# Performance work log

Measured on AMD Instinct MI355X. Metric: run time of the kernel, lower is better.

Reference implementation:

```python
import jax, jax.numpy as jnp
import numpy as np

N, E, D, H, C = 100000, 1600000, 64, 8, 10
NEG_SLOPE = 0.2


def setup_inputs() -> dict:
    key = jax.random.key(0)
    ks = jax.random.split(key, 20)
    rn = lambda k, sh: jax.random.normal(k, sh, jnp.float32) * 0.1
    return dict(
        x=jax.random.normal(ks[0], (N, D), jnp.float32),
        edge_index=jax.random.randint(ks[1], (2, E), 0, N),
        gcnK_W=rn(ks[2], (D, D)), gcnK_b=rn(ks[3], (D,)),
        gcnV_W=rn(ks[4], (D, D)), gcnV_b=rn(ks[5], (D,)),
        super_Q=rn(ks[6], (C, D)),
        mha_in_w=rn(ks[7], (3 * D, D)), mha_in_b=rn(ks[8], (3 * D,)),
        mha_out_w=rn(ks[9], (D, D)), mha_out_b=rn(ks[10], (D,)),
        gat_W=rn(ks[11], (D, D)), gat_Wc=rn(ks[12], (D, D)),
        gat_a_src=rn(ks[13], (D,)), gat_a_dst=rn(ks[14], (D,)),
        gat_b=rn(ks[15], (D,)),
        t1_W=rn(ks[16], (D, 2 * D)), t1_b=rn(ks[17], (2 * D,)),
        t2_W=rn(ks[18], (2 * D, D)), t2_b=rn(ks[19], (D,)),
    )


def _gcn(x, W, b, src, dst, norm_e):
    # PyG GCNConv: symmetric-normalized aggregation over (A + I)
    h = x @ W  # [N, D]
    agg = jax.ops.segment_sum(h[src] * norm_e[:, None], dst, num_segments=N)
    return agg + b


def _mha(q, k, v, in_w, in_b, out_w, out_b):
    # torch.nn.MultiheadAttention (unbatched), eval mode (dropout off)
    L, n, hd = q.shape[0], k.shape[0], D // H
    Wq, Wk, Wv = jnp.split(in_w, 3, axis=0)
    bq, bk, bv = jnp.split(in_b, 3)
    scale = 1.0 / float(np.sqrt(hd))
    qh = ((q @ Wq.T + bq) * scale).reshape(L, H, hd).transpose(1, 0, 2)  # [H,L,hd]
    kh = (k @ Wk.T + bk).reshape(n, H, hd).transpose(1, 0, 2)            # [H,n,hd]
    vh = (v @ Wv.T + bv).reshape(n, H, hd).transpose(1, 0, 2)
    attn = jax.nn.softmax(jnp.einsum('hld,hnd->hln', qh, kh), axis=-1)
    o = jnp.einsum('hln,hnd->hld', attn, vh).transpose(1, 0, 2).reshape(L, D)
    return o @ out_w.T + out_b


def _context_gat(x, src, dst, context, W, Wc, a_src, a_dst, b):
    # context-conditioned GAT: per-edge logits use node terms + global context gate
    h = x @ W
    c = context @ Wc  # [D]
    s_src = h @ (a_src + c)  # context modulates source attention vector
    s_dst = h @ a_dst
    logits = jax.nn.leaky_relu(s_src[src] + s_dst[dst], NEG_SLOPE)  # [E]
    m = jax.ops.segment_max(logits, dst, num_segments=N)
    ex = jnp.exp(logits - m[dst])
    denom = jax.ops.segment_sum(ex, dst, num_segments=N)
    alpha = ex / (denom[dst] + 1e-16)
    out = jax.ops.segment_sum(alpha[:, None] * h[src], dst, num_segments=N)
    return out + b


def reference(x, edge_index, gcnK_W, gcnK_b, gcnV_W, gcnV_b, super_Q,
              mha_in_w, mha_in_b, mha_out_w, mha_out_b,
              gat_W, gat_Wc, gat_a_src, gat_a_dst, gat_b,
              t1_W, t1_b, t2_W, t2_b):
    src, dst = edge_index[0], edge_index[1]
    loop = jnp.arange(N)
    srcl = jnp.concatenate([src, loop])
    dstl = jnp.concatenate([dst, loop])
    deg = jax.ops.segment_sum(jnp.ones_like(srcl, jnp.float32), dstl, num_segments=N)
    dinv = jnp.where(deg > 0, 1.0 / jnp.sqrt(deg), 0.0)
    norm_e = dinv[srcl] * dinv[dstl]
    x_K = _gcn(x, gcnK_W, gcnK_b, srcl, dstl, norm_e)
    x_V = _gcn(x, gcnV_W, gcnV_b, srcl, dstl, norm_e)
    cluster = _mha(super_Q, x_K, x_V, mha_in_w, mha_in_b, mha_out_w, mha_out_b)  # [C, D]
    context = jnp.mean(cluster, axis=0)  # [D]
    g = _context_gat(x_V, src, dst, context, gat_W, gat_Wc, gat_a_src, gat_a_dst, gat_b)
    h1 = jax.nn.relu(g @ t1_W + t1_b)
    return jax.nn.relu(h1 @ t2_W + t2_b)
```

## Files before the change

### kernel.cpp

```cpp
#include <hip/hip_runtime.h>
#include <hip/hip_bf16.h>
#include <stdint.h>

#define NN 100000
#define EE 1600000
#define NBK 391
#define CHUNK 4096
#define NCB 98
#define NPROJ 1563
#define NS 32

typedef __attribute__((ext_vector_type(8))) short bf16x8;
typedef __attribute__((ext_vector_type(4))) float f32x4;
typedef __attribute__((ext_vector_type(2))) float f32x2;
union FragU { uint4 u; bf16x8 h; };

__device__ inline unsigned pack_bf2(float a, float b) {
  __hip_bfloat162 t;
  t.x = __float2bfloat16(a);
  t.y = __float2bfloat16(b);
  return *reinterpret_cast<unsigned*>(&t);
}

__device__ inline f32x2 unpk2(unsigned u) {
  f32x2 r;
  r.x = __uint_as_float(u << 16);
  r.y = __uint_as_float(u & 0xffff0000u);
  return r;
}

__launch_bounds__(256)
__global__ void k_hist(const int* __restrict__ ei, int* __restrict__ histmat) {
  __shared__ int hist[NCB];
  int t = threadIdx.x;
  if (t < NCB) hist[t] = 0;
  __syncthreads();
  int base = blockIdx.x * CHUNK;
  int nb = EE - base; if (nb > CHUNK) nb = CHUNK;
  for (int k = t; k < nb; k += 256)
    atomicAdd(&hist[ei[EE + base + k] >> 10], 1);
  __syncthreads();
  if (t < NCB) histmat[blockIdx.x * NCB + t] = hist[t];
}

__launch_bounds__(256)
__global__ void k_sumcb(const int* __restrict__ histmat, int* __restrict__ cbsum) {
  __shared__ int red[4];
  int cb = blockIdx.x, t = threadIdx.x;
  int s = 0;
  for (int blk = t; blk < NBK; blk += 256) s += histmat[blk * NCB + cb];
#pragma unroll
  for (int off = 32; off > 0; off >>= 1) s += __shfl_down(s, off);
  if ((t & 63) == 0) red[t >> 6] = s;
  __syncthreads();
  if (t == 0) cbsum[cb] = red[0] + red[1] + red[2] + red[3];
}

__launch_bounds__(512)
__global__ void k_ppos(const int* __restrict__ histmat, const int* __restrict__ cbsum,
                       int* __restrict__ bstart, int* __restrict__ offsets,
                       int* __restrict__ ppos) {
  __shared__ int sm[512];
  __shared__ int sb[128];
  int cb = blockIdx.x, t = threadIdx.x;
  if (t < 128) sb[t] = (t < NCB) ? cbsum[t] : 0;
  __syncthreads();
  for (int off = 1; off < 128; off <<= 1) {
    int x = (t < 128 && t >= off) ? sb[t - off] : 0;
    __syncthreads();
    if (t < 128) sb[t] += x;
    __syncthreads();
  }
  int bs = (cb == 0) ? 0 : sb[cb - 1];
  if (t == 0) bstart[cb] = bs;
  if (cb == 0 && t == 0) { bstart[NCB] = EE; offsets[NN] = EE; }
  int v = (t < NBK) ? histmat[t * NCB + cb] : 0;
  sm[t] = v;
  __syncthreads();
  for (int off = 1; off < 512; off <<= 1) {
    int x = (t >= off) ? sm[t - off] : 0;
    __syncthreads();
    sm[t] += x;
    __syncthreads();
  }
  if (t < NBK) ppos[cb * NBK + t] = bs + sm[t] - v;
}

__launch_bounds__(256)
__global__ void k_fill_b(const int* __restrict__ ei, const int* __restrict__ ppos,
                         unsigned* __restrict__ brec) {
  __shared__ int hist[NCB], binstart[NCB], bincur[NCB], pbase[NCB];
  __shared__ unsigned lbuf[CHUNK];
  __shared__ unsigned char cbArr[CHUNK];
  int t = threadIdx.x;
  int base = blockIdx.x * CHUNK;
  int nb = EE - base; if (nb > CHUNK) nb = CHUNK;
  if (t < NCB) { hist[t] = 0; pbase[t] = ppos[t * NBK + blockIdx.x]; }
  __syncthreads();
  unsigned rec[16]; int rcb[16]; int cnt = 0;
  for (int k = t; k < nb; k += 256) {
    int s = ei[base + k], d = ei[EE + base + k];
    rec[cnt] = (unsigned)s | ((unsigned)(d & 1023) << 17);
    rcb[cnt] = d >> 10;
    atomicAdd(&hist[rcb[cnt]], 1);
    cnt++;
  }
  __syncthreads();
  if (t < NCB) binstart[t] = hist[t];
  __syncthreads();
  for (int off = 1; off < NCB; off <<= 1) {
    int v = (t < NCB && t >= off) ? binstart[t - off] : 0;
    __syncthreads();
    if (t < NCB) binstart[t] += v;
    __syncthreads();
  }
  if (t < NCB) { binstart[t] -= hist[t]; bincur[t] = 0; }
  __syncthreads();
  for (int i = 0; i < cnt; i++) {
    int c = rcb[i];
    int pos = atomicAdd(&bincur[c], 1);
    int p = binstart[c] + pos;
    lbuf[p] = rec[i];
    cbArr[p] = (unsigned char)c;
  }
  __syncthreads();
  for (int i = t; i < nb; i += 256) {
    int c = cbArr[i];
    brec[pbase[c] + (i - binstart[c])] = lbuf[i];
  }
}

__launch_bounds__(1024)
__global__ void k_fill_c(const unsigned* __restrict__ brec, const int* __restrict__ bstart,
                         int* __restrict__ csr, int* __restrict__ offsets,
                         float* __restrict__ dinv) {
  __shared__ int cnt[1024], sm[1024];
  int cbk = blockIdx.x, t = threadIdx.x;
  int nb0 = cbk << 10;
  int nn = NN - nb0; if (nn > 1024) nn = 1024;
  cnt[t] = 0;
  __syncthreads();
  int e0 = bstart[cbk], e1 = bstart[cbk + 1];
  for (int j = e0 + t; j < e1; j += 1024)
    atomicAdd(&cnt[brec[j] >> 17], 1);
  __syncthreads();
  int cv = cnt[t];
  sm[t] = cv;
  __syncthreads();
  for (int off = 1; off < 1024; off <<= 1) {
    int v = (t >= off) ? sm[t - off] : 0;
    __syncthreads();
    sm[t] += v;
    __syncthreads();
  }
  sm[t] -= cv;
  if (t < nn) {
    offsets[nb0 + t] = e0 + sm[t];
    dinv[nb0 + t] = rsqrtf((float)(cv + 1));
  }
  cnt[t] = 0;
  __syncthreads();
  for (int j = e0 + t; j < e1; j += 1024) {
    unsigned r = brec[j];
    int dl = r >> 17;
    int p = atomicAdd(&cnt[dl], 1);
    csr[e0 + sm[dl] + p] = r & 0x1FFFF;
  }
}

__global__ void k_prep(const float* __restrict__ x, const float* __restrict__ dinv,
                       unsigned* __restrict__ xbf2) {
  int i = blockIdx.x * 256 + threadIdx.x;
  if (i >= NN * 32) return;
  float dv = dinv[i >> 5];
  float2 v = ((const float2*)x)[i];
  xbf2[i] = pack_bf2(v.x * dv, v.y * dv);
}

__launch_bounds__(256)
__global__ void k_agg_x(const unsigned* __restrict__ xbf2, const int* __restrict__ offsets,
                        const int* __restrict__ csr, const float* __restrict__ dinv,
                        unsigned* __restrict__ axb) {
  int gid = blockIdx.x * 256 + threadIdx.x;
  int n = gid >> 6;
  if (n >= NN) return;
  int lane = gid & 63, q = lane & 7, grp = lane >> 3;
  int e0 = offsets[n], e1 = offsets[n + 1];
  float dv = dinv[n];
  f32x2 a2[4];
#pragma unroll
  for (int i = 0; i < 4; i++) a2[i] = (f32x2){0.f, 0.f};
  if (grp == 0) {
    uint4 u = ((const uint4*)(xbf2 + (size_t)n * 32))[q];
    unsigned uu[4] = {u.x, u.y, u.z, u.w};
#pragma unroll
    for (int p = 0; p < 4; p++) a2[p] += unpk2(uu[p]);
  }
  int b2 = e0;
  for (; b2 + 8 < e1; b2 += 16) {
    int j0 = b2 + grp, j1 = j0 + 8;
    int s0 = csr[j0];
    bool ok1 = j1 < e1;
    int s1 = ok1 ? csr[j1] : s0;
    uint4 u0 = ((const uint4*)(xbf2 + (size_t)s0 * 32))[q];
    uint4 u1 = ((const uint4*)(xbf2 + (size_t)s1 * 32))[q];
    unsigned w0[4] = {u0.x, u0.y, u0.z, u0.w};
    unsigned w1[4] = {u1.x, u1.y, u1.z, u1.w};
#pragma unroll
    for (int p = 0; p < 4; p++) a2[p] += unpk2(w0[p]);
    if (ok1) {
#pragma unroll
      for (int p = 0; p < 4; p++) a2[p] += unpk2(w1[p]);
    }
  }
  for (; b2 < e1; b2 += 8) {
    int j = b2 + grp;
    if (j < e1) {
      int s = csr[j];
      uint4 u = ((const uint4*)(xbf2 + (size_t)s * 32))[q];
      unsigned uu[4] = {u.x, u.y, u.z, u.w};
#pragma unroll
      for (int p = 0; p < 4; p++) a2[p] += unpk2(uu[p]);
    }
  }
#pragma unroll
  for (int i = 0; i < 4; i++) {
    a2[i].x += __shfl_xor(a2[i].x, 8);
    a2[i].x += __shfl_xor(a2[i].x, 16);
    a2[i].x += __shfl_xor(a2[i].x, 32);
    a2[i].y += __shfl_xor(a2[i].y, 8);
    a2[i].y += __shfl_xor(a2[i].y, 16);
    a2[i].y += __shfl_xor(a2[i].y, 32);
  }
  if (lane < 8) {
    uint4 u;
    u.x = pack_bf2(a2[0].x * dv, a2[0].y * dv);
    u.y = pack_bf2(a2[1].x * dv, a2[1].y * dv);
    u.z = pack_bf2(a2[2].x * dv, a2[2].y * dv);
    u.w = pack_bf2(a2[3].x * dv, a2[3].y * dv);
    ((uint4*)(axb + (size_t)n * 32))[q] = u;
  }
}

__launch_bounds__(256)
__global__ void k_fusew(const float* __restrict__ gcnK_W, const float* __restrict__ gcnK_b,
                        const float* __restrict__ gcnV_W, const float* __restrict__ gcnV_b,
                        const float* __restrict__ mha_in_w, const float* __restrict__ mha_in_b,
                        const float* __restrict__ gat_W, const float* __restrict__ sQ,
                        const float* __restrict__ t1W, const float* __restrict__ t2W,
                        unsigned* __restrict__ Wt, float* __restrict__ bb,
                        unsigned* __restrict__ W1b, unsigned* __restrict__ W2b) {
  __shared__ float sW1[64 * 65];
  __shared__ float sW2[64 * 65];
  __shared__ float sW3[64 * 65];
  __shared__ float sqq[640], qhs[640], Ms[5120], kb[64];
  int blk = blockIdx.x, t = threadIdx.x;
  const float scale = 0.35355339059327373f;
  if (blk < 16) {
    for (int i = t; i < 4096; i += 256) sW1[(i >> 6) * 65 + (i & 63)] = gcnV_W[i];
    if (blk < 8) {
      for (int i = t; i < 512; i += 256) sW2[i] = mha_in_w[(128 + blk * 8) * 64 + i];
    } else {
      for (int i = t; i < 4096; i += 256) sW2[(i >> 6) * 65 + (i & 63)] = gat_W[i];
    }
    __syncthreads();
    int idx = blk * 256 + t;
    int d = idx >> 5, kp = idx & 31;
    float v2[2];
#pragma unroll
    for (int u2 = 0; u2 < 2; u2++) {
      int k = kp * 2 + u2;
      float s = 0.f;
      if (d < 64) {
        int r = d & 7;
        for (int j = 0; j < 64; j++) s = fmaf(sW1[k * 65 + j], sW2[r * 64 + j], s);
      } else {
        int c = d - 64;
        for (int j = 0; j < 64; j++) s = fmaf(sW1[k * 65 + j], sW2[j * 65 + c], s);
      }
      v2[u2] = s;
    }
    Wt[idx] = pack_bf2(v2[0], v2[1]);
    if (t < 8) {
      if (blk < 8) {
        int d0 = blk * 8 + t;
        float s = mha_in_b[128 + d0];
        for (int j = 0; j < 64; j++) s = fmaf(gcnV_b[j], sW2[t * 64 + j], s);
        bb[d0] = s;
      } else {
        int c = (blk - 8) * 8 + t;
        float s = 0.f;
        for (int j = 0; j < 64; j++) s = fmaf(gcnV_b[j], sW2[j * 65 + c], s);
        bb[64 + c] = s;
      }
    }
  } else if (blk == 16) {
    for (int i = t; i < 4096; i += 256) {
      int r = i >> 6, c = i & 63;
      sW1[r * 65 + c] = gcnK_W[i];
      sW2[r * 65 + c] = mha_in_w[64 * 64 + i];
      sW3[r * 65 + c] = mha_in_w[i];
    }
    for (int i = t; i < 640; i += 256) sqq[i] = sQ[i];
    __syncthreads();
    for (int e = t; e < 640; e += 256) {
      int lv = e >> 6, c = e & 63;
      float acc = mha_in_b[c];
      for (int i = 0; i < 64; i++) acc = fmaf(sqq[lv * 64 + i], sW3[c * 65 + i], acc);
      qhs[e] = acc * scale;
    }
    if (t < 64) {
      float s = mha_in_b[64 + t];
      for (int j = 0; j < 64; j++) s = fmaf(gcnK_b[j], sW2[t * 65 + j], s);
      kb[t] = s;
    }
    __syncthreads();
    for (int e = t; e < 5120; e += 256) {
      int j = e / 80, hl = e % 80;
      int h = hl / 10, lv = hl % 10;
      float s = 0.f;
#pragma unroll
      for (int c = 0; c < 8; c++) {
        int cp = h * 8 + c;
        s = fmaf(sW2[cp * 65 + j], qhs[lv * 64 + cp], s);
      }
      Ms[j * 80 + hl] = s;
    }
    if (t < 80) {
      int h = t / 10, lv = t % 10;
      float s = 0.f;
#pragma unroll
      for (int c = 0; c < 8; c++) {
        int cp = h * 8 + c;
        s = fmaf(kb[cp], qhs[lv * 64 + cp], s);
      }
      bb[128 + t] = s;
    }
    __syncthreads();
    for (int e = t; e < 2560; e += 256) {
      int hl = e >> 5, kp = e & 31;
      float v2[2];
#pragma unroll
      for (int u2 = 0; u2 < 2; u2++) {
        int k = kp * 2 + u2;
        float s = 0.f;
        for (int j = 0; j < 64; j++) s = fmaf(sW1[k * 65 + j], Ms[j * 80 + hl], s);
        v2[u2] = s;
      }
      Wt[(128 + hl) * 32 + kp] = pack_bf2(v2[0], v2[1]);
    }
  } else if (blk < 33) {
    int idx = (blk - 17) * 256 + t;
    int col = idx >> 5, kp = idx & 31;
    W1b[idx] = pack_bf2(t1W[(2 * kp) * 128 + col], t1W[(2 * kp + 1) * 128 + col]);
  } else {
    int idx = (blk - 33) * 256 + t;
    int col = idx >> 6, kp = idx & 63;
    W2b[idx] = pack_bf2(t2W[(2 * kp) * 64 + col], t2W[(2 * kp + 1) * 64 + col]);
  }
}

__launch_bounds__(256)
__global__ void k_proj(const unsigned* __restrict__ axb, const unsigned* __restrict__ Wt,
                       const float* __restrict__ bb, const float* __restrict__ a_dst,
                       unsigned char* __restrict__ hG8,
                       float* __restrict__ s_dstv, float* __restrict__ part2) {
  __shared__ float red[4][720];
  int t = threadIdx.x;
  int wid = t >> 6, l = t & 63;
  int l15 = l & 15, lg = l >> 4;
  int base = blockIdx.x * 64;
  int rowbase = base + wid * 16;

  FragU a0, a1;
  {
    int r = rowbase + l15;
    if (r < NN) {
      const uint4* p = (const uint4*)(axb + (size_t)r * 32);
      a0.u = p[lg];
      a1.u = p[4 + lg];
    } else {
      a0.u = make_uint4(0u, 0u, 0u, 0u);
      a1.u = a0.u;
    }
  }
  f32x4 acc[13];
#pragma unroll
  for (int ct = 0; ct < 13; ct++) acc[ct] = (f32x4){0.f, 0.f, 0.f, 0.f};
#pragma unroll
  for (int ct = 0; ct < 13; ct++) {
    const uint4* wp = (const uint4*)(Wt + (size_t)(ct * 16 + l15) * 32);
    FragU b0, b1;
    b0.u = wp[lg];
    b1.u = wp[4 + lg];
    acc[ct] = __builtin_amdgcn_mfma_f32_16x16x32_bf16(a0.h, b0.h, acc[ct], 0, 0, 0);
    acc[ct] = __builtin_amdgcn_mfma_f32_16x16x32_bf16(a1.h, b1.h, acc[ct], 0, 0, 0);
  }

  float sdp[4] = {0.f, 0.f, 0.f, 0.f};
#pragma unroll
  for (int gt = 0; gt < 4; gt++) {
    int col = gt * 16 + l15;
    float bias = bb[64 + col];
    float ad = a_dst[col];
#pragma unroll
    for (int r = 0; r < 4; r++) {
      float hg = acc[4 + gt][r] + bias;
      sdp[r] = fmaf(hg, ad, sdp[r]);
      int row = rowbase + lg * 4 + r;
      if (row < NN) {
        unsigned wq = __builtin_amdgcn_cvt_pk_fp8_f32(hg, hg, 0u, false);
        hG8[(size_t)row * 64 + col] = (unsigned char)(wq & 0xffu);
      }
    }
  }
#pragma unroll
  for (int r = 0; r < 4; r++) {
    float v = sdp[r];
    v += __shfl_xor(v, 1); v += __shfl_xor(v, 2);
    v += __shfl_xor(v, 4); v += __shfl_xor(v, 8);
    int row = rowbase + lg * 4 + r;
    if (l15 == 0 && row < NN) s_dstv[row] = v;
  }

  float wz[5][4];
#pragma unroll
  for (int zt = 0; zt < 5; zt++) {
    int zcol = zt * 16 + l15;
    float bias = bb[128 + zcol];
    float sp = 0.f;
#pragma unroll
    for (int r = 0; r < 4; r++) {
      int row = rowbase + lg * 4 + r;
      float z = acc[8 + zt][r] + bias;
      float w = (row < NN) ? __expf(z) : 0.f;
      wz[zt][r] = w;
      sp += w;
    }
    sp += __shfl_xor(sp, 16);
    sp += __shfl_xor(sp, 32);
    if (l < 16) {
      int h = zcol / 10, lv = zcol % 10;
      red[wid][h * 90 + lv] = sp;
    }
  }

  int sA = (l15 + 32 * lg) & 63;
  int sB2 = (sA + 16) & 63;
  bool loK = (lg < 2);
  FragU af[5];
#pragma unroll
  for (int zt = 0; zt < 5; zt++) {
    unsigned wlo = pack_bf2(wz[zt][0], wz[zt][1]);
    unsigned whi = pack_bf2(wz[zt][2], wz[zt][3]);
    unsigned f0 = __shfl(wlo, sA), f1 = __shfl(whi, sA);
    unsigned f2 = __shfl(wlo, sB2), f3 = __shfl(whi, sB2);
    af[zt].u.x = loK ? f0 : 0u;
    af[zt].u.y = loK ? f1 : 0u;
    af[zt].u.z = loK ? f2 : 0u;
    af[zt].u.w = loK ? f3 : 0u;
  }
#pragma unroll
  for (int vt = 0; vt < 4; vt++) {
    float bias = bb[vt * 16 + l15];
    unsigned vlo = pack_bf2(acc[vt][0] + bias, acc[vt][1] + bias);
    unsigned vhi = pack_bf2(acc[vt][2] + bias, acc[vt][3] + bias);
    FragU bf;
    {
      unsigned f0 = __shfl(vlo, sA), f1 = __shfl(vhi, sA);
      unsigned f2 = __shfl(vlo, sB2), f3 = __shfl(vhi, sB2);
      bf.u.x = loK ? f0 : 0u;
      bf.u.y = loK ? f1 : 0u;
      bf.u.z = loK ? f2 : 0u;
      bf.u.w = loK ? f3 : 0u;
    }
    f32x4 oacc[5];
#pragma unroll
    for (int zt = 0; zt < 5; zt++) {
      oacc[zt] = (f32x4){0.f, 0.f, 0.f, 0.f};
      oacc[zt] = __builtin_amdgcn_mfma_f32_16x16x32_bf16(af[zt].h, bf.h, oacc[zt], 0, 0, 0);
    }
#pragma unroll
    for (int zt = 0; zt < 5; zt++) {
#pragma unroll
      for (int r = 0; r < 4; r++) {
        int hl = zt * 16 + lg * 4 + r;
        int h = hl / 10, lv = hl - h * 10;
        if (vt * 2 + (l15 >> 3) == h)
          red[wid][h * 90 + 10 + lv * 8 + (l15 & 7)] = oacc[zt][r];
      }
    }
  }

  __syncthreads();
  float* p2 = part2 + (size_t)(blockIdx.x & (NS - 1)) * 720;
  for (int j = t; j < 720; j += 256) {
    float v = red[0][j] + red[1][j] + red[2][j] + red[3][j];
    atomicAdd(&p2[j], v);
  }
}

__global__ void k_context(const float* __restrict__ part2, const float* __restrict__ out_w,
                          const float* __restrict__ out_b, const float* __restrict__ a_src,
                          const float* __restrict__ gat_Wc, float* __restrict__ aeff) {
  __shared__ float po[640], cl[640], ctx[64], ac[720];
  int t = threadIdx.x;
  for (int j = t; j < 720; j += 640) {
    float v = 0.f;
#pragma unroll
    for (int s = 0; s < NS; s++) v += part2[(size_t)s * 720 + j];
    int cg = j / 90, r = j % 90;
    ac[(r < 10) ? (cg * 10 + r) : (80 + cg * 80 + (r - 10))] = v;
  }
  __syncthreads();
  {
    int h = t / 80, r = t % 80, l = r >> 3, j = r & 7;
    po[l * 64 + h * 8 + j] = ac[80 + t] / ac[h * 10 + l];
  }
  __syncthreads();
  {
    int l = t >> 6, d = t & 63;
    float v = out_b[d];
    for (int c = 0; c < 64; c++) v = fmaf(po[l * 64 + c], out_w[d * 64 + c], v);
    cl[t] = v;
  }
  __syncthreads();
  if (t < 64) {
    float m = 0.f;
#pragma unroll
    for (int l = 0; l < 10; l++) m += cl[l * 64 + t];
    ctx[t] = m * 0.1f;
  }
  __syncthreads();
  if (t < 64) {
    float v = a_src[t];
    for (int i = 0; i < 64; i++) v = fmaf(ctx[i], gat_Wc[i * 64 + t], v);
    aeff[t] = v;
  }
}

__launch_bounds__(256)
__global__ void k_ssrc(const unsigned char* __restrict__ hG8, const float* __restrict__ aeff,
                       float* __restrict__ s_src) {
  int gid = blockIdx.x * 256 + threadIdx.x;
  int n = gid >> 6, lane = gid & 63;
  if (n >= NN) return;
  unsigned b = hG8[(size_t)n * 64 + lane];
  float v = __builtin_amdgcn_cvt_f32_fp8(b, 0) * aeff[lane];
#pragma unroll
  for (int off = 32; off > 0; off >>= 1) v += __shfl_xor(v, off);
  if (lane == 0) s_src[n] = v;
}

__launch_bounds__(256)
__global__ void k_gat(const int* __restrict__ offsets, const int* __restrict__ csr,
                      const float* __restrict__ s_src, const float* __restrict__ s_dstv,
                      const unsigned char* __restrict__ hG8, const float* __restrict__ gat_b,
                      unsigned* __restrict__ gb) {
  int gid = blockIdx.x * 256 + threadIdx.x;
  int n = gid >> 6;
  if (n >= NN) return;
  int lane = gid & 63, q = lane & 7, grp = lane >> 3;
  int e0 = offsets[n], e1 = offsets[n + 1];
  float sd = s_dstv[n];
  float den = 0.f;
  f32x2 a2[4];
#pragma unroll
  for (int i = 0; i < 4; i++) a2[i] = (f32x2){0.f, 0.f};
  int b2 = e0;
  for (; b2 + 8 < e1; b2 += 16) {
    int j0 = b2 + grp, j1 = j0 + 8;
    int s0 = csr[j0];
    bool ok1 = j1 < e1;
    int s1 = ok1 ? csr[j1] : s0;
    float z0 = s_src[s0] + sd;
    float z1 = s_src[s1] + sd;
    uint2 u0 = ((const uint2*)(hG8 + (size_t)s0 * 64))[q];
    uint2 u1 = ((const uint2*)(hG8 + (size_t)s1 * 64))[q];
    z0 = z0 > 0.f ? z0 : 0.2f * z0;
    float ex0 = __expf(z0);
    den += ex0;
    f32x2 e0v = (f32x2){ex0, ex0};
    {
      f32x2 p0 = __builtin_amdgcn_cvt_pk_f32_fp8(u0.x, false);
      f32x2 p1 = __builtin_amdgcn_cvt_pk_f32_fp8(u0.x, true);
      f32x2 p2 = __builtin_amdgcn_cvt_pk_f32_fp8(u0.y, false);
      f32x2 p3 = __builtin_amdgcn_cvt_pk_f32_fp8(u0.y, true);
      a2[0] = e0v * p0 + a2[0];
      a2[1] = e0v * p1 + a2[1];
      a2[2] = e0v * p2 + a2[2];
      a2[3] = e0v * p3 + a2[3];
    }
    if (ok1) {
      z1 = z1 > 0.f ? z1 : 0.2f * z1;
      float ex1 = __expf(z1);
      den += ex1;
      f32x2 e1v = (f32x2){ex1, ex1};
      f32x2 p0 = __builtin_amdgcn_cvt_pk_f32_fp8(u1.x, false);
      f32x2 p1 = __builtin_amdgcn_cvt_pk_f32_fp8(u1.x, true);
      f32x2 p2 = __builtin_amdgcn_cvt_pk_f32_fp8(u1.y, false);
      f32x2 p3 = __builtin_amdgcn_cvt_pk_f32_fp8(u1.y, true);
      a2[0] = e1v * p0 + a2[0];
      a2[1] = e1v * p1 + a2[1];
      a2[2] = e1v * p2 + a2[2];
      a2[3] = e1v * p3 + a2[3];
    }
  }
  for (; b2 < e1; b2 += 8) {
    int j = b2 + grp;
    if (j < e1) {
      int s = csr[j];
      float z = s_src[s] + sd;
      z = z > 0.f ? z : 0.2f * z;
      float ex = __expf(z);
      den += ex;
      uint2 u = ((const uint2*)(hG8 + (size_t)s * 64))[q];
      f32x2 ev = (f32x2){ex, ex};
      f32x2 p0 = __builtin_amdgcn_cvt_pk_f32_fp8(u.x, false);
      f32x2 p1 = __builtin_amdgcn_cvt_pk_f32_fp8(u.x, true);
      f32x2 p2 = __builtin_amdgcn_cvt_pk_f32_fp8(u.y, false);
      f32x2 p3 = __builtin_amdgcn_cvt_pk_f32_fp8(u.y, true);
      a2[0] = ev * p0 + a2[0];
      a2[1] = ev * p1 + a2[1];
      a2[2] = ev * p2 + a2[2];
      a2[3] = ev * p3 + a2[3];
    }
  }
  den += __shfl_xor(den, 8);
  den += __shfl_xor(den, 16);
  den += __shfl_xor(den, 32);
#pragma unroll
  for (int i = 0; i < 4; i++) {
    a2[i].x += __shfl_xor(a2[i].x, 8);
    a2[i].x += __shfl_xor(a2[i].x, 16);
    a2[i].x += __shfl_xor(a2[i].x, 32);
    a2[i].y += __shfl_xor(a2[i].y, 8);
    a2[i].y += __shfl_xor(a2[i].y, 16);
    a2[i].y += __shfl_xor(a2[i].y, 32);
  }
  float inv = 1.f / (den + 1e-16f);
  if (lane < 8) {
    uint4 u;
    u.x = pack_bf2(a2[0].x * inv + gat_b[q * 8 + 0], a2[0].y * inv + gat_b[q * 8 + 1]);
    u.y = pack_bf2(a2[1].x * inv + gat_b[q * 8 + 2], a2[1].y * inv + gat_b[q * 8 + 3]);
    u.z = pack_bf2(a2[2].x * inv + gat_b[q * 8 + 4], a2[2].y * inv + gat_b[q * 8 + 5]);
    u.w = pack_bf2(a2[3].x * inv + gat_b[q * 8 + 6], a2[3].y * inv + gat_b[q * 8 + 7]);
    ((uint4*)(gb + (size_t)n * 32))[q] = u;
  }
}

__launch_bounds__(256)
__global__ void k_mlp1(const unsigned* __restrict__ gb, const unsigned* __restrict__ W1b,
                       const float* __restrict__ b1, unsigned* __restrict__ h1b) {
  int t = threadIdx.x;
  int wid = t >> 6, l = t & 63;
  int l15 = l & 15, lg = l >> 4;
  int rowbase = blockIdx.x * 64 + wid * 16;
  FragU a0, a1;
  {
    int r = rowbase + l15;
    if (r < NN) {
      const uint4* p = (const uint4*)(gb + (size_t)r * 32);
      a0.u = p[lg];
      a1.u = p[4 + lg];
    } else {
      a0.u = make_uint4(0u, 0u, 0u, 0u);
      a1.u = a0.u;
    }
  }
  f32x4 acc[8];
#pragma unroll
  for (int ct = 0; ct < 8; ct++) acc[ct] = (f32x4){0.f, 0.f, 0.f, 0.f};
#pragma unroll
  for (int ct = 0; ct < 8; ct++) {
    const uint4* wp = (const uint4*)(W1b + (size_t)(ct * 16 + l15) * 32);
    FragU b0, b1f;
    b0.u = wp[lg];
    b1f.u = wp[4 + lg];
    acc[ct] = __builtin_amdgcn_mfma_f32_16x16x32_bf16(a0.h, b0.h, acc[ct], 0, 0, 0);
    acc[ct] = __builtin_amdgcn_mfma_f32_16x16x32_bf16(a1.h, b1f.h, acc[ct], 0, 0, 0);
  }
  __hip_bfloat16* hp = (__hip_bfloat16*)h1b;
#pragma unroll
  for (int ct = 0; ct < 8; ct++) {
    int col = ct * 16 + l15;
    float bias = b1[col];
#pragma unroll
    for (int r = 0; r < 4; r++) {
      int row = rowbase + lg * 4 + r;
      if (row < NN) hp[(size_t)row * 128 + col] = __float2bfloat16(fmaxf(acc[ct][r] + bias, 0.f));
    }
  }
}

__launch_bounds__(256)
__global__ void k_mlp2(const unsigned* __restrict__ h1b, const unsigned* __restrict__ W2b,
                       const float* __restrict__ b2, float* __restrict__ out) {
  int t = threadIdx.x;
  int wid = t >> 6, l = t & 63;
  int l15 = l & 15, lg = l >> 4;
  int rowbase = blockIdx.x * 64 + wid * 16;
  FragU a[4];
  {
    int r = rowbase + l15;
    if (r < NN) {
      const uint4* p = (const uint4*)(h1b + (size_t)r * 64);
#pragma unroll
      for (int ks = 0; ks < 4; ks++) a[ks].u = p[4 * ks + lg];
    } else {
#pragma unroll
      for (int ks = 0; ks < 4; ks++) a[ks].u = make_uint4(0u, 0u, 0u, 0u);
    }
  }
  f32x4 acc[4];
#pragma unroll
  for (int ct = 0; ct < 4; ct++) acc[ct] = (f32x4){0.f, 0.f, 0.f, 0.f};
#pragma unroll
  for (int ct = 0; ct < 4; ct++) {
    const uint4* wp = (const uint4*)(W2b + (size_t)(ct * 16 + l15) * 64);
#pragma unroll
    for (int ks = 0; ks < 4; ks++) {
      FragU bf;
      bf.u = wp[4 * ks + lg];
      acc[ct] = __builtin_amdgcn_mfma_f32_16x16x32_bf16(a[ks].h, bf.h, acc[ct], 0, 0, 0);
    }
  }
#pragma unroll
  for (int ct = 0; ct < 4; ct++) {
    int col = ct * 16 + l15;
    float bias = b2[col];
#pragma unroll
    for (int r = 0; r < 4; r++) {
      int row = rowbase + lg * 4 + r;
      if (row < NN) out[(size_t)row * 64 + col] = fmaxf(acc[ct][r] + bias, 0.f);
    }
  }
}

extern "C" void kernel_launch(void* const* d_in, const int* in_sizes, int n_in,
                              void* d_out, int out_size, void* d_ws, size_t ws_size,
                              hipStream_t stream) {
  (void)in_sizes; (void)n_in; (void)out_size; (void)ws_size;
  const float* x        = (const float*)d_in[0];
  const int*   ei       = (const int*)d_in[1];
  const float* gcnK_W   = (const float*)d_in[2];
  const float* gcnK_b   = (const float*)d_in[3];
  const float* gcnV_W   = (const float*)d_in[4];
  const float* gcnV_b   = (const float*)d_in[5];
  const float* super_Q  = (const float*)d_in[6];
  const float* mha_in_w = (const float*)d_in[7];
  const float* mha_in_b = (const float*)d_in[8];
  const float* mha_out_w= (const float*)d_in[9];
  const float* mha_out_b= (const float*)d_in[10];
  const float* gat_W    = (const float*)d_in[11];
  const float* gat_Wc   = (const float*)d_in[12];
  const float* gat_a_src= (const float*)d_in[13];
  const float* gat_a_dst= (const float*)d_in[14];
  const float* gat_b    = (const float*)d_in[15];
  const float* t1_W     = (const float*)d_in[16];
  const float* t1_b     = (const float*)d_in[17];
  const float* t2_W     = (const float*)d_in[18];
  const float* t2_b     = (const float*)d_in[19];

  char* ws = (char*)d_ws;
  size_t cur = 0;
  auto alloc = [&](size_t bytes) -> char* {
    char* p = ws + cur;
    cur = (cur + bytes + 255) & ~(size_t)255;
    return p;
  };
  int*      histmat = (int*)alloc((size_t)NBK * NCB * 4);
  int*      cbsum   = (int*)alloc((size_t)NCB * 4);
  int*      ppos    = (int*)alloc((size_t)NCB * NBK * 4);
  int*      bstart  = (int*)alloc((size_t)(NCB + 1) * 4);
  int*      offsets = (int*)alloc((size_t)(NN + 1) * 4);
  float*    dinv    = (float*)alloc((size_t)NN * 4);
  int*      csr     = (int*)alloc((size_t)EE * 4);
  unsigned* brec    = (unsigned*)alloc((size_t)EE * 4);
  unsigned* Wt      = (unsigned*)alloc((size_t)208 * 32 * 4);
  float*    bb      = (float*)alloc(208 * 4);
  unsigned* W1b     = (unsigned*)alloc((size_t)4096 * 4);
  unsigned* W2b     = (unsigned*)alloc((size_t)4096 * 4);
  float*    aeff    = (float*)alloc(64 * 4);
  float*    part2   = (float*)alloc((size_t)NS * 720 * 4);
  float*    s_src   = (float*)alloc((size_t)NN * 4);
  float*    s_dstv  = (float*)alloc((size_t)NN * 4);
  unsigned* xbf     = (unsigned*)alloc((size_t)NN * 128);
  unsigned* axb     = (unsigned*)alloc((size_t)NN * 128);
  unsigned char* hG8 = (unsigned char*)alloc((size_t)NN * 64);
  unsigned* gb      = (unsigned*)alloc((size_t)NN * 128);
  unsigned* h1b     = (unsigned*)alloc((size_t)NN * 64 * 4);
  float*    g       = (float*)d_out;

  hipMemsetAsync(part2, 0, (size_t)NS * 720 * 4, stream);
  k_hist<<<NBK, 256, 0, stream>>>(ei, histmat);
  k_sumcb<<<NCB, 256, 0, stream>>>(histmat, cbsum);
  k_ppos<<<NCB, 512, 0, stream>>>(histmat, cbsum, bstart, offsets, ppos);
  k_fill_b<<<NBK, 256, 0, stream>>>(ei, ppos, brec);
  k_fill_c<<<NCB, 1024, 0, stream>>>(brec, bstart, csr, offsets, dinv);
  k_prep<<<(NN * 32 + 255) / 256, 256, 0, stream>>>(x, dinv, xbf);
  k_agg_x<<<NN / 4, 256, 0, stream>>>(xbf, offsets, csr, dinv, axb);
  k_fusew<<<49, 256, 0, stream>>>(gcnK_W, gcnK_b, gcnV_W, gcnV_b, mha_in_w, mha_in_b,
                                  gat_W, super_Q, t1_W, t2_W, Wt, bb, W1b, W2b);
  k_proj<<<NPROJ, 256, 0, stream>>>(axb, Wt, bb, gat_a_dst, hG8, s_dstv, part2);
  k_context<<<1, 640, 0, stream>>>(part2, mha_out_w, mha_out_b, gat_a_src, gat_Wc, aeff);
  k_ssrc<<<NN / 4, 256, 0, stream>>>(hG8, aeff, s_src);
  k_gat<<<NN / 4, 256, 0, stream>>>(offsets, csr, s_src, s_dstv, hG8, gat_b, gb);
  k_mlp1<<<(NN + 63) / 64, 256, 0, stream>>>(gb, W1b, t1_b, h1b);
  k_mlp2<<<(NN + 63) / 64, 256, 0, stream>>>(h1b, W2b, t2_b, g);
}
```

Before: 376.6 us.

## Fuse MLP layers via LDS, fold prep into CSR fill and sumcb into ppos

The two MLP kernels are merged so the hidden activations stay in shared memory instead of being written to and re-read from a global bf16 buffer. The x scaling/bf16 packing is moved into the CSR fill kernel, and the per-bucket column sums are computed inside the prefix-position kernel. This removes three launches and a large intermediate buffer. In exchange, each ppos block redundantly does a serial 391-step sum, and the fill kernel takes on extra work at low block count.

```diff
diff --git a/kernel.cpp b/kernel.cpp
--- a/kernel.cpp
+++ b/kernel.cpp
@@ -43,27 +43,20 @@
   if (t < NCB) histmat[blockIdx.x * NCB + t] = hist[t];
 }
 
-__launch_bounds__(256)
-__global__ void k_sumcb(const int* __restrict__ histmat, int* __restrict__ cbsum) {
-  __shared__ int red[4];
-  int cb = blockIdx.x, t = threadIdx.x;
-  int s = 0;
-  for (int blk = t; blk < NBK; blk += 256) s += histmat[blk * NCB + cb];
-#pragma unroll
-  for (int off = 32; off > 0; off >>= 1) s += __shfl_down(s, off);
-  if ((t & 63) == 0) red[t >> 6] = s;
-  __syncthreads();
-  if (t == 0) cbsum[cb] = red[0] + red[1] + red[2] + red[3];
-}
-
 __launch_bounds__(512)
-__global__ void k_ppos(const int* __restrict__ histmat, const int* __restrict__ cbsum,
+__global__ void k_ppos(const int* __restrict__ histmat,
                        int* __restrict__ bstart, int* __restrict__ offsets,
                        int* __restrict__ ppos) {
   __shared__ int sm[512];
   __shared__ int sb[128];
   int cb = blockIdx.x, t = threadIdx.x;
-  if (t < 128) sb[t] = (t < NCB) ? cbsum[t] : 0;
+  if (t < 128) {
+    int s = 0;
+    if (t < NCB) {
+      for (int blk = 0; blk < NBK; blk++) s += histmat[blk * NCB + t];
+    }
+    sb[t] = s;
+  }
   __syncthreads();
   for (int off = 1; off < 128; off <<= 1) {
     int x = (t < 128 && t >= off) ? sb[t - off] : 0;
@@ -133,7 +126,8 @@
 __launch_bounds__(1024)
 __global__ void k_fill_c(const unsigned* __restrict__ brec, const int* __restrict__ bstart,
                          int* __restrict__ csr, int* __restrict__ offsets,
-                         float* __restrict__ dinv) {
+                         float* __restrict__ dinv,
+                         const float* __restrict__ x, unsigned* __restrict__ xbf2) {
   __shared__ int cnt[1024], sm[1024];
   int cbk = blockIdx.x, t = threadIdx.x;
   int nb0 = cbk << 10;
@@ -154,9 +148,10 @@
     __syncthreads();
   }
   sm[t] -= cv;
+  float dvmine = rsqrtf((float)(cv + 1));
   if (t < nn) {
     offsets[nb0 + t] = e0 + sm[t];
-    dinv[nb0 + t] = rsqrtf((float)(cv + 1));
+    dinv[nb0 + t] = dvmine;
   }
   cnt[t] = 0;
   __syncthreads();
@@ -166,15 +161,14 @@
     int p = atomicAdd(&cnt[dl], 1);
     csr[e0 + sm[dl] + p] = r & 0x1FFFF;
   }
-}
-
-__global__ void k_prep(const float* __restrict__ x, const float* __restrict__ dinv,
-                       unsigned* __restrict__ xbf2) {
-  int i = blockIdx.x * 256 + threadIdx.x;
-  if (i >= NN * 32) return;
-  float dv = dinv[i >> 5];
-  float2 v = ((const float2*)x)[i];
-  xbf2[i] = pack_bf2(v.x * dv, v.y * dv);
+  __syncthreads();
+  int npairs = nn * 32;
+  for (int idx = t; idx < npairs; idx += 1024) {
+    int i = nb0 * 32 + idx;
+    float dv = dinv[nb0 + (idx >> 5)];
+    float2 v = ((const float2*)x)[i];
+    xbf2[i] = pack_bf2(v.x * dv, v.y * dv);
+  }
 }
 
 __launch_bounds__(256)
@@ -650,8 +644,10 @@
 }
 
 __launch_bounds__(256)
-__global__ void k_mlp1(const unsigned* __restrict__ gb, const unsigned* __restrict__ W1b,
-                       const float* __restrict__ b1, unsigned* __restrict__ h1b) {
+__global__ void k_mlp(const unsigned* __restrict__ gb, const unsigned* __restrict__ W1b,
+                      const float* __restrict__ b1, const unsigned* __restrict__ W2b,
+                      const float* __restrict__ b2, float* __restrict__ out) {
+  __shared__ unsigned short sh[4][16][136];
   int t = threadIdx.x;
   int wid = t >> 6, l = t & 63;
   int l15 = l & 15, lg = l >> 4;
@@ -668,53 +664,36 @@
       a1.u = a0.u;
     }
   }
-  f32x4 acc[8];
-#pragma unroll
-  for (int ct = 0; ct < 8; ct++) acc[ct] = (f32x4){0.f, 0.f, 0.f, 0.f};
+  f32x4 acc1[8];
+#pragma unroll
+  for (int ct = 0; ct < 8; ct++) acc1[ct] = (f32x4){0.f, 0.f, 0.f, 0.f};
 #pragma unroll
   for (int ct = 0; ct < 8; ct++) {
     const uint4* wp = (const uint4*)(W1b + (size_t)(ct * 16 + l15) * 32);
     FragU b0, b1f;
     b0.u = wp[lg];
     b1f.u = wp[4 + lg];
-    acc[ct] = __builtin_amdgcn_mfma_f32_16x16x32_bf16(a0.h, b0.h, acc[ct], 0, 0, 0);
-    acc[ct] = __builtin_amdgcn_mfma_f32_16x16x32_bf16(a1.h, b1f.h, acc[ct], 0, 0, 0);
-  }
-  __hip_bfloat16* hp = (__hip_bfloat16*)h1b;
+    acc1[ct] = __builtin_amdgcn_mfma_f32_16x16x32_bf16(a0.h, b0.h, acc1[ct], 0, 0, 0);
+    acc1[ct] = __builtin_amdgcn_mfma_f32_16x16x32_bf16(a1.h, b1f.h, acc1[ct], 0, 0, 0);
+  }
 #pragma unroll
   for (int ct = 0; ct < 8; ct++) {
     int col = ct * 16 + l15;
     float bias = b1[col];
 #pragma unroll
     for (int r = 0; r < 4; r++) {
-      int row = rowbase + lg * 4 + r;
-      if (row < NN) hp[(size_t)row * 128 + col] = __float2bfloat16(fmaxf(acc[ct][r] + bias, 0.f));
-    }
-  }
-}
-
-__launch_bounds__(256)
-__global__ void k_mlp2(const unsigned* __restrict__ h1b, const unsigned* __restrict__ W2b,
-                       const float* __restrict__ b2, float* __restrict__ out) {
-  int t = threadIdx.x;
-  int wid = t >> 6, l = t & 63;
-  int l15 = l & 15, lg = l >> 4;
-  int rowbase = blockIdx.x * 64 + wid * 16;
+      float h = fmaxf(acc1[ct][r] + bias, 0.f);
+      sh[wid][lg * 4 + r][col] = (unsigned short)(pack_bf2(h, 0.f) & 0xffffu);
+    }
+  }
+  __syncthreads();
   FragU a[4];
-  {
-    int r = rowbase + l15;
-    if (r < NN) {
-      const uint4* p = (const uint4*)(h1b + (size_t)r * 64);
-#pragma unroll
-      for (int ks = 0; ks < 4; ks++) a[ks].u = p[4 * ks + lg];
-    } else {
-#pragma unroll
-      for (int ks = 0; ks < 4; ks++) a[ks].u = make_uint4(0u, 0u, 0u, 0u);
-    }
-  }
-  f32x4 acc[4];
-#pragma unroll
-  for (int ct = 0; ct < 4; ct++) acc[ct] = (f32x4){0.f, 0.f, 0.f, 0.f};
+#pragma unroll
+  for (int ks = 0; ks < 4; ks++)
+    a[ks].u = *(const uint4*)&sh[wid][l15][ks * 32 + lg * 8];
+  f32x4 acc2[4];
+#pragma unroll
+  for (int ct = 0; ct < 4; ct++) acc2[ct] = (f32x4){0.f, 0.f, 0.f, 0.f};
 #pragma unroll
   for (int ct = 0; ct < 4; ct++) {
     const uint4* wp = (const uint4*)(W2b + (size_t)(ct * 16 + l15) * 64);
@@ -722,7 +701,7 @@
     for (int ks = 0; ks < 4; ks++) {
       FragU bf;
       bf.u = wp[4 * ks + lg];
-      acc[ct] = __builtin_amdgcn_mfma_f32_16x16x32_bf16(a[ks].h, bf.h, acc[ct], 0, 0, 0);
+      acc2[ct] = __builtin_amdgcn_mfma_f32_16x16x32_bf16(a[ks].h, bf.h, acc2[ct], 0, 0, 0);
     }
   }
 #pragma unroll
@@ -732,7 +711,7 @@
 #pragma unroll
     for (int r = 0; r < 4; r++) {
       int row = rowbase + lg * 4 + r;
-      if (row < NN) out[(size_t)row * 64 + col] = fmaxf(acc[ct][r] + bias, 0.f);
+      if (row < NN) out[(size_t)row * 64 + col] = fmaxf(acc2[ct][r] + bias, 0.f);
     }
   }
 }
@@ -770,7 +749,6 @@
     return p;
   };
   int*      histmat = (int*)alloc((size_t)NBK * NCB * 4);
-  int*      cbsum   = (int*)alloc((size_t)NCB * 4);
   int*      ppos    = (int*)alloc((size_t)NCB * NBK * 4);
   int*      bstart  = (int*)alloc((size_t)(NCB + 1) * 4);
   int*      offsets = (int*)alloc((size_t)(NN + 1) * 4);
@@ -789,16 +767,13 @@
   unsigned* axb     = (unsigned*)alloc((size_t)NN * 128);
   unsigned char* hG8 = (unsigned char*)alloc((size_t)NN * 64);
   unsigned* gb      = (unsigned*)alloc((size_t)NN * 128);
-  unsigned* h1b     = (unsigned*)alloc((size_t)NN * 64 * 4);
   float*    g       = (float*)d_out;
 
   hipMemsetAsync(part2, 0, (size_t)NS * 720 * 4, stream);
   k_hist<<<NBK, 256, 0, stream>>>(ei, histmat);
-  k_sumcb<<<NCB, 256, 0, stream>>>(histmat, cbsum);
-  k_ppos<<<NCB, 512, 0, stream>>>(histmat, cbsum, bstart, offsets, ppos);
+  k_ppos<<<NCB, 512, 0, stream>>>(histmat, bstart, offsets, ppos);
   k_fill_b<<<NBK, 256, 0, stream>>>(ei, ppos, brec);
-  k_fill_c<<<NCB, 1024, 0, stream>>>(brec, bstart, csr, offsets, dinv);
-  k_prep<<<(NN * 32 + 255) / 256, 256, 0, stream>>>(x, dinv, xbf);
+  k_fill_c<<<NCB, 1024, 0, stream>>>(brec, bstart, csr, offsets, dinv, x, xbf);
   k_agg_x<<<NN / 4, 256, 0, stream>>>(xbf, offsets, csr, dinv, axb);
   k_fusew<<<49, 256, 0, stream>>>(gcnK_W, gcnK_b, gcnV_W, gcnV_b, mha_in_w, mha_in_b,
                                   gat_W, super_Q, t1_W, t2_W, Wt, bb, W1b, W2b);
@@ -806,6 +781,5 @@
   k_context<<<1, 640, 0, stream>>>(part2, mha_out_w, mha_out_b, gat_a_src, gat_Wc, aeff);
   k_ssrc<<<NN / 4, 256, 0, stream>>>(hG8, aeff, s_src);
   k_gat<<<NN / 4, 256, 0, stream>>>(offsets, csr, s_src, s_dstv, hG8, gat_b, gb);
-  k_mlp1<<<(NN + 63) / 64, 256, 0, stream>>>(gb, W1b, t1_b, h1b);
-  k_mlp2<<<(NN + 63) / 64, 256, 0, stream>>>(h1b, W2b, t2_b, g);
-}
+  k_mlp<<<(NN + 63) / 64, 256, 0, stream>>>(gb, W1b, t1_b, W2b, t2_b, g);
+}
```

Measured after the change: 381.1 us. No clear change (+1.2%).
